# Kernel optimization log

Measured on AMD Instinct MI355X. Metric: run time of the kernel, lower is better.

The kernel has to match this reference:

```python
import jax, jax.numpy as jnp
import numpy as np

N_A = 100000
N_B = 100000


def _mean_agg(x_src, src, dst, n_dst):
    # gather source features along edges, mean-aggregate into destination nodes
    msgs = x_src[src]                                        # [E, d]
    s = jax.ops.segment_sum(msgs, dst, num_segments=n_dst)   # [n_dst, d]
    ones = jnp.ones((dst.shape[0], 1), dtype=x_src.dtype)
    cnt = jax.ops.segment_sum(ones, dst, num_segments=n_dst)
    return s / jnp.maximum(cnt, jnp.asarray(1.0, x_src.dtype))


def setup_inputs() -> dict:
    key = jax.random.key(0)
    ks = jax.random.split(key, 13)
    E = 1200000
    d = 64
    return {
        "x_A": jax.random.normal(ks[0], (N_A, d), jnp.float32),
        "x_B": jax.random.normal(ks[1], (N_B, d), jnp.float32),
        "Wn": jax.random.normal(ks[2], (2, 3, d, d), jnp.float32) * 0.1,
        "Wr": jax.random.normal(ks[3], (2, 3, d, d), jnp.float32) * 0.1,
        "b": jax.random.normal(ks[4], (2, 3, d), jnp.float32) * 0.1,
        "W_out": jax.random.normal(ks[5], (d, d), jnp.float32) * 0.1,
        "b_out": jax.random.normal(ks[6], (d,), jnp.float32) * 0.1,
        "src0": jax.random.randint(ks[7], (E,), 0, N_A, jnp.int64 if jax.config.jax_enable_x64 else jnp.int32),
        "dst0": jax.random.randint(ks[8], (E,), 0, N_B, jnp.int32),
        "src1": jax.random.randint(ks[9], (E,), 0, N_B, jnp.int32),
        "dst1": jax.random.randint(ks[10], (E,), 0, N_A, jnp.int32),
        "src2": jax.random.randint(ks[11], (E,), 0, N_A, jnp.int32),
        "dst2": jax.random.randint(ks[12], (E,), 0, N_A, jnp.int32),
    }


def reference(x_A, x_B, Wn, Wr, b, W_out, b_out,
              src0, dst0, src1, dst1, src2, dst2):
    # Two stacked heterogeneous conv layers (SAGEConv-style per edge type,
    # summed across edge types per destination node type), then Linear+ReLU head.
    for l in range(2):
        m0 = _mean_agg(x_A, src0, dst0, N_B)  # A -> B
        m1 = _mean_agg(x_B, src1, dst1, N_A)  # B -> A
        m2 = _mean_agg(x_A, src2, dst2, N_A)  # A -> A
        new_B = m0 @ Wn[l, 0] + x_B @ Wr[l, 0] + b[l, 0]
        new_A = (m1 @ Wn[l, 1] + x_A @ Wr[l, 1] + b[l, 1]
                 + m2 @ Wn[l, 2] + x_A @ Wr[l, 2] + b[l, 2])
        x_A, x_B = new_A, new_B
    out_A = jax.nn.relu(x_A @ W_out + b_out)
    out_B = jax.nn.relu(x_B @ W_out + b_out)
    return jnp.concatenate([out_A, out_B], axis=0)  # [N_A + N_B, d]
```

## Files before the change

kernel.cpp:

```cpp
#include <hip/hip_runtime.h>
#include <hip/hip_bf16.h>

typedef __bf16 bf16_t;
typedef unsigned short u16;
typedef short short8 __attribute__((ext_vector_type(8)));
typedef float f32x4 __attribute__((ext_vector_type(4)));

#define BSHIFT 9
#define CAP 8192
#define TILE 8192

__device__ inline short f2bs(float v) {
    bf16_t h = (bf16_t)v;
    return __builtin_bit_cast(short, h);
}
__device__ inline float uif(unsigned u) { return __builtin_bit_cast(float, u); }

__global__ __launch_bounds__(256) void prep_convert(
    const float* __restrict__ xA, const float* __restrict__ xB,
    const float* __restrict__ Wn, const float* __restrict__ Wr,
    const float* __restrict__ Wout, const float* __restrict__ b,
    const float* __restrict__ b_out,
    u16* __restrict__ plane0, u16* __restrict__ wh,
    int* __restrict__ gcursor, float* __restrict__ biasC,
    int NA, int NB, int K) {
    int nA4 = NA * 16, nB4 = NB * 16;
    int bA = (nA4 + 255) / 256, bB = (nB4 + 255) / 256;
    int bi = blockIdx.x;
    int tid = threadIdx.x;
    if (bi < bA + bB) {
        const float* in = (bi < bA) ? xA : xB;
        u16* out = (bi < bA) ? plane0 : plane0 + (size_t)NA * 64;
        int i = (bi < bA ? bi : bi - bA) * 256 + tid;
        int n4 = (bi < bA) ? nA4 : nB4;
        if (i >= n4) return;
        float4 v = ((const float4*)in)[i];
        u16 o[4];
        o[0] = (u16)f2bs(v.x); o[1] = (u16)f2bs(v.y);
        o[2] = (u16)f2bs(v.z); o[3] = (u16)f2bs(v.w);
        *(uint2*)(out + (size_t)i * 4) = *(uint2*)o;
        return;
    }
    if (bi < bA + bB + 11) {
        int mat = bi - bA - bB;
        u16* dstp = wh + (size_t)mat * 4096;
        for (int i = tid; i < 4096; i += 256) {
            int k = i >> 6, n = i & 63;
            float v;
            if (mat < 6) v = Wn[(size_t)mat * 4096 + i];
            else if (mat < 8) v = Wr[(size_t)((mat - 6) * 3 + 0) * 4096 + i];
            else if (mat < 10) v = Wr[(size_t)((mat - 8) * 3 + 1) * 4096 + i]
                                 + Wr[(size_t)((mat - 8) * 3 + 2) * 4096 + i];
            else v = Wout[i];
            dstp[n * 64 + k] = (u16)f2bs(v);
        }
        return;
    }
    if (bi < bA + bB + 11 + 5) {
        int c = bi - bA - bB - 11;
        const float* Wsrc;
        const float* Wsrc2 = nullptr;
        if (c == 0) Wsrc = Wn + (size_t)3 * 4096;
        else if (c == 1) Wsrc = Wr + (size_t)3 * 4096;
        else if (c == 2) Wsrc = Wn + (size_t)4 * 4096;
        else if (c == 3) Wsrc = Wn + (size_t)5 * 4096;
        else { Wsrc = Wr + (size_t)4 * 4096; Wsrc2 = Wr + (size_t)5 * 4096; }
        __shared__ float Ws[64 * 64];
        __shared__ float Wo[64 * 64];
        for (int i = tid; i < 4096; i += 256) {
            float w = Wsrc[i];
            if (Wsrc2) w += Wsrc2[i];
            Ws[i] = w;
            Wo[i] = Wout[i];
        }
        __syncthreads();
        u16* dstp = wh + (size_t)(11 + c) * 4096;
        for (int it = 0; it < 16; ++it) {
            int i = it * 256 + tid;
            int k = i >> 6, n = i & 63;
            float s0 = 0.f, s1 = 0.f, s2 = 0.f, s3 = 0.f;
#pragma unroll
            for (int j = 0; j < 64; j += 4) {
                s0 += Ws[k * 64 + j]     * Wo[j * 64 + n];
                s1 += Ws[k * 64 + j + 1] * Wo[(j + 1) * 64 + n];
                s2 += Ws[k * 64 + j + 2] * Wo[(j + 2) * 64 + n];
                s3 += Ws[k * 64 + j + 3] * Wo[(j + 3) * 64 + n];
            }
            dstp[n * 64 + k] = (u16)f2bs((s0 + s1) + (s2 + s3));
        }
        return;
    }
    for (int i = tid; i < K; i += 256) gcursor[i] = i * CAP;
    if (tid < 64) {
        int n = tid;
        float s0 = b_out[n], s1 = b_out[n];
        for (int j = 0; j < 64; j++) {
            float wo = Wout[j * 64 + n];
            s0 += b[3 * 64 + j] * wo;
            s1 += (b[4 * 64 + j] + b[5 * 64 + j]) * wo;
        }
        biasC[0 * 64 + n] = b[0 * 64 + n];
        biasC[1 * 64 + n] = b[1 * 64 + n] + b[2 * 64 + n];
        biasC[2 * 64 + n] = s0;
        biasC[3 * 64 + n] = s1;
    }
}

__global__ __launch_bounds__(1024) void partition_kernel(
    const int* __restrict__ s0, const int* __restrict__ d0,
    const int* __restrict__ s1, const int* __restrict__ d1,
    const int* __restrict__ s2, const int* __restrict__ d2,
    int* __restrict__ gcursor, int* __restrict__ pairs,
    int NB, int NA, int E, int total) {
    __shared__ int hist[1024];
    __shared__ int gbase[1024];
    int tid = threadIdx.x;
    for (int tile = blockIdx.x * TILE; tile < total; tile += gridDim.x * TILE) {
        hist[tid] = 0;
        __syncthreads();
        int mybkt[8], mypk[8], myrank[8];
#pragma unroll
        for (int j = 0; j < 8; j++) {
            int idx = tile + j * 1024 + tid;
            int g = -1, s = 0;
            if (idx < total) {
                if (idx < E) { s = s0[idx]; g = d0[idx]; }
                else if (idx < 2 * E) { s = s1[idx - E]; g = NB + d1[idx - E]; }
                else { s = s2[idx - 2 * E]; g = NB + NA + d2[idx - 2 * E]; }
            }
            if (g >= 0) {
                mybkt[j] = g >> BSHIFT;
                mypk[j] = ((g & ((1 << BSHIFT) - 1)) << 17) | s;
                myrank[j] = atomicAdd(&hist[mybkt[j]], 1);
            } else mybkt[j] = -1;
        }
        __syncthreads();
        {
            int c = hist[tid];
            if (c) gbase[tid] = atomicAdd(&gcursor[tid], c);
        }
        __syncthreads();
#pragma unroll
        for (int j = 0; j < 8; j++) {
            if (mybkt[j] >= 0)
                pairs[gbase[mybkt[j]] + myrank[j]] = mypk[j];
        }
        __syncthreads();
    }
}

__global__ __launch_bounds__(512) void bucket_fill(const int* __restrict__ pairs,
                                                   const int* __restrict__ gcursor,
                                                   int* __restrict__ off_s,
                                                   int* __restrict__ off_e,
                                                   int* __restrict__ colidx, int M) {
    int b = blockIdx.x;
    int gb = b << BSHIFT;
    __shared__ int cnt[512], cur[512], wsum[8];
    int tid = threadIdx.x;
    int lane = tid & 63, w = tid >> 6;
    int p0 = b * CAP, p1 = gcursor[b];
    cnt[tid] = 0;
    __syncthreads();
    for (int e = p0 + tid; e < p1; e += 512)
        atomicAdd(&cnt[(unsigned)pairs[e] >> 17], 1);
    __syncthreads();
    int v = cnt[tid];
    int x = v;
#pragma unroll
    for (int off = 1; off < 64; off <<= 1) {
        int n = __shfl_up(x, off);
        if (lane >= off) x += n;
    }
    if (lane == 63) wsum[w] = x;
    __syncthreads();
    if (tid == 0) {
        int s = 0;
#pragma unroll
        for (int i = 0; i < 8; i++) { int t = wsum[i]; wsum[i] = s; s += t; }
    }
    __syncthreads();
    int excl = x - v + wsum[w];
    cur[tid] = excl;
    int g = gb + tid;
    if (g < M) { off_s[g] = p0 + excl; off_e[g] = p0 + excl + v; }
    __syncthreads();
    for (int e = p0 + tid; e < p1; e += 512) {
        int p = pairs[e];
        int pos = atomicAdd(&cur[(unsigned)p >> 17], 1);
        colidx[p0 + pos] = p & 0x1FFFF;
    }
}

__device__ __forceinline__ void acc8(uint4 u, f32x4& a0, f32x4& a1) {
    a0[0] += uif(u.x << 16); a0[1] += uif(u.x & 0xFFFF0000u);
    a0[2] += uif(u.y << 16); a0[3] += uif(u.y & 0xFFFF0000u);
    a1[0] += uif(u.z << 16); a1[1] += uif(u.z & 0xFFFF0000u);
    a1[2] += uif(u.w << 16); a1[3] += uif(u.w & 0xFFFF0000u);
}

__device__ __forceinline__ uint4 gather_seg(const char* __restrict__ tab,
                                            const int* __restrict__ colidx,
                                            int s0, int s1, unsigned fo) {
    f32x4 a0 = {0.f, 0.f, 0.f, 0.f}, a1 = {0.f, 0.f, 0.f, 0.f};
    int e = s0;
    if (e + 3 < s1) {
        int c0 = colidx[e], c1 = colidx[e + 1];
        int c2 = colidx[e + 2], c3 = colidx[e + 3];
        while (e + 7 < s1) {
            uint4 u0 = *(const uint4*)(tab + (((unsigned)c0 << 7) | fo));
            uint4 u1 = *(const uint4*)(tab + (((unsigned)c1 << 7) | fo));
            uint4 u2 = *(const uint4*)(tab + (((unsigned)c2 << 7) | fo));
            uint4 u3 = *(const uint4*)(tab + (((unsigned)c3 << 7) | fo));
            c0 = colidx[e + 4]; c1 = colidx[e + 5];
            c2 = colidx[e + 6]; c3 = colidx[e + 7];
            acc8(u0, a0, a1); acc8(u1, a0, a1);
            acc8(u2, a0, a1); acc8(u3, a0, a1);
            e += 4;
        }
        {
            uint4 u0 = *(const uint4*)(tab + (((unsigned)c0 << 7) | fo));
            uint4 u1 = *(const uint4*)(tab + (((unsigned)c1 << 7) | fo));
            uint4 u2 = *(const uint4*)(tab + (((unsigned)c2 << 7) | fo));
            uint4 u3 = *(const uint4*)(tab + (((unsigned)c3 << 7) | fo));
            acc8(u0, a0, a1); acc8(u1, a0, a1);
            acc8(u2, a0, a1); acc8(u3, a0, a1);
            e += 4;
        }
    }
    for (; e < s1; ++e) {
        int c = colidx[e];
        uint4 u = *(const uint4*)(tab + (((unsigned)c << 7) | fo));
        acc8(u, a0, a1);
    }
    float inv = 1.0f / fmaxf((float)(s1 - s0), 1.0f);
    u16 o[8];
#pragma unroll
    for (int i = 0; i < 4; i++) o[i] = (u16)f2bs(a0[i] * inv);
#pragma unroll
    for (int i = 0; i < 4; i++) o[4 + i] = (u16)f2bs(a1[i] * inv);
    return *(uint4*)o;
}

template <int L2>
__global__ __launch_bounds__(256) void fused_layer(
    const u16* __restrict__ plane_in, void* __restrict__ outv,
    const int* __restrict__ colidx,
    const int* __restrict__ off_s, const int* __restrict__ off_e,
    const u16* __restrict__ wh, const float* __restrict__ biasC,
    int NA, int NB, int blocksBf) {
    __shared__ __align__(16) u16 mS[32][72];
    const int tid = threadIdx.x;
    const int w = tid >> 6, lane = tid & 63;
    const int oct = lane >> 3, fl = lane & 7;
    const unsigned fo = (unsigned)(fl << 4);
    const char* pA = (const char*)plane_in;
    const char* pB = (const char*)(plane_in + (size_t)NA * 64);
    const int r = lane & 15, q = lane >> 4;
    short8 zf;
#pragma unroll
    for (int j = 0; j < 8; j++) zf[j] = 0;

    if ((int)blockIdx.x < blocksBf) {
        const int row0 = blockIdx.x * 32;
        const int rt = w >> 1;
        const int tbase = (w & 1) * 2;
        const int arow = row0 + rt * 16 + r;
        const bool av = arow < NB;
        short8 ax0 = av ? *(const short8*)(pB + (size_t)arow * 128 + q * 16) : zf;
        short8 ax1 = av ? *(const short8*)(pB + (size_t)arow * 128 + 64 + q * 16) : zf;
        {
            int seg = w * 8 + oct;
            int brow = row0 + seg;
            int s0 = 0, s1 = 0;
            if (brow < NB) { s0 = off_s[brow]; s1 = off_e[brow]; }
            uint4 mv = gather_seg(pA, colidx, s0, s1, fo);
            *(uint4*)&mS[seg][fl * 8] = mv;
        }
        __syncthreads();
        const u16* WmT = wh + (size_t)(L2 ? 11 : 0) * 4096;
        const u16* WxT = wh + (size_t)(L2 ? 12 : 6) * 4096;
        const float* bb = biasC + (size_t)(L2 ? 2 : 0) * 64;
        f32x4 acc[2];
#pragma unroll
        for (int t2 = 0; t2 < 2; t2++) {
            float bv = bb[(tbase + t2) * 16 + r];
            acc[t2][0] = bv; acc[t2][1] = bv; acc[t2][2] = bv; acc[t2][3] = bv;
        }
#pragma unroll
        for (int ks = 0; ks < 2; ks++) {
            short8 am = *(const short8*)&mS[rt * 16 + r][ks * 32 + q * 8];
            short8 ax = ks ? ax1 : ax0;
#pragma unroll
            for (int t2 = 0; t2 < 2; t2++) {
                size_t widx = (size_t)((tbase + t2) * 16 + r) * 64 + ks * 32 + q * 8;
                acc[t2] = __builtin_amdgcn_mfma_f32_16x16x32_bf16(am, *(const short8*)(WmT + widx), acc[t2], 0, 0, 0);
                acc[t2] = __builtin_amdgcn_mfma_f32_16x16x32_bf16(ax, *(const short8*)(WxT + widx), acc[t2], 0, 0, 0);
            }
        }
#pragma unroll
        for (int t2 = 0; t2 < 2; t2++) {
            int col = (tbase + t2) * 16 + r;
#pragma unroll
            for (int rr = 0; rr < 4; rr++) {
                int row = row0 + rt * 16 + q * 4 + rr;
                if (row < NB) {
                    float v = acc[t2][rr];
                    if (L2) __builtin_nontemporal_store(fmaxf(v, 0.0f),
                                (float*)outv + (size_t)(NA + row) * 64 + col);
                    else ((u16*)outv)[(size_t)(NA + row) * 64 + col] = (u16)f2bs(v);
                }
            }
        }
    } else {
        const int row0 = ((int)blockIdx.x - blocksBf) * 16;
        const int t = w;
        const int arow = row0 + r;
        const bool av = arow < NA;
        short8 ax0 = av ? *(const short8*)(pA + (size_t)arow * 128 + q * 16) : zf;
        short8 ax1 = av ? *(const short8*)(pA + (size_t)arow * 128 + 64 + q * 16) : zf;
        {
            int seg = w * 8 + oct;
            int rrow = row0 + (seg & 15);
            bool m2 = seg >= 16;
            int s0 = 0, s1 = 0;
            if (rrow < NA) {
                int g = m2 ? (NB + NA + rrow) : (NB + rrow);
                s0 = off_s[g]; s1 = off_e[g];
            }
            uint4 mv = gather_seg(m2 ? pA : pB, colidx, s0, s1, fo);
            *(uint4*)&mS[seg][fl * 8] = mv;
        }
        __syncthreads();
        const u16* Wm1T = wh + (size_t)(L2 ? 13 : 1) * 4096;
        const u16* Wm2T = wh + (size_t)(L2 ? 14 : 2) * 4096;
        const u16* WxT  = wh + (size_t)(L2 ? 15 : 8) * 4096;
        const float* bb = biasC + (size_t)(L2 ? 3 : 1) * 64;
        f32x4 acc;
        {
            float bv = bb[t * 16 + r];
            acc[0] = bv; acc[1] = bv; acc[2] = bv; acc[3] = bv;
        }
#pragma unroll
        for (int ks = 0; ks < 2; ks++) {
            short8 am1 = *(const short8*)&mS[r][ks * 32 + q * 8];
            short8 am2 = *(const short8*)&mS[16 + r][ks * 32 + q * 8];
            short8 ax = ks ? ax1 : ax0;
            size_t widx = (size_t)(t * 16 + r) * 64 + ks * 32 + q * 8;
            acc = __builtin_amdgcn_mfma_f32_16x16x32_bf16(am1, *(const short8*)(Wm1T + widx), acc, 0, 0, 0);
            acc = __builtin_amdgcn_mfma_f32_16x16x32_bf16(am2, *(const short8*)(Wm2T + widx), acc, 0, 0, 0);
            acc = __builtin_amdgcn_mfma_f32_16x16x32_bf16(ax, *(const short8*)(WxT + widx), acc, 0, 0, 0);
        }
        {
            int col = t * 16 + r;
#pragma unroll
            for (int rr = 0; rr < 4; rr++) {
                int row = row0 + q * 4 + rr;
                if (row < NA) {
                    float v = acc[rr];
                    if (L2) __builtin_nontemporal_store(fmaxf(v, 0.0f),
                                (float*)outv + (size_t)row * 64 + col);
                    else ((u16*)outv)[(size_t)row * 64 + col] = (u16)f2bs(v);
                }
            }
        }
    }
}

extern "C" void kernel_launch(void* const* d_in, const int* in_sizes, int n_in,
                              void* d_out, int out_size, void* d_ws, size_t ws_size,
                              hipStream_t stream) {
    const float* xA_in = (const float*)d_in[0];
    const float* xB_in = (const float*)d_in[1];
    const float* Wn = (const float*)d_in[2];
    const float* Wr = (const float*)d_in[3];
    const float* b = (const float*)d_in[4];
    const float* W_out = (const float*)d_in[5];
    const float* b_out = (const float*)d_in[6];
    const int* src0 = (const int*)d_in[7];
    const int* dst0 = (const int*)d_in[8];
    const int* src1 = (const int*)d_in[9];
    const int* dst1 = (const int*)d_in[10];
    const int* src2 = (const int*)d_in[11];
    const int* dst2 = (const int*)d_in[12];

    const int NA = in_sizes[0] / 64;
    const int NB = in_sizes[1] / 64;
    const int E = in_sizes[7];
    const int M = NB + NA + NA;
    const int total = 3 * E;
    const int K = (M + (1 << BSHIFT) - 1) >> BSHIFT;

    const size_t PL = (size_t)(NA + NB) * 64;
    u16* plane[2];
    plane[0] = (u16*)d_ws;
    plane[1] = plane[0] + PL;
    u16* wh     = plane[1] + PL;
    int* gcursor= (int*)(wh + 16 * 4096);
    float* biasC= (float*)(gcursor + 1024);
    int* off_s  = (int*)(biasC + 256);
    int* off_e  = off_s + M;
    int* colidx = off_e + M;
    int* pairs  = colidx + (size_t)K * CAP;

    int bA = (NA * 16 + 255) / 256, bB = (NB * 16 + 255) / 256;
    prep_convert<<<bA + bB + 11 + 5 + 1, 256, 0, stream>>>(
        xA_in, xB_in, Wn, Wr, W_out, b, b_out,
        plane[0], wh, gcursor, biasC, NA, NB, K);

    int ntiles = (total + TILE - 1) / TILE;
    partition_kernel<<<ntiles, 1024, 0, stream>>>(src0, dst0, src1, dst1, src2, dst2,
                                                  gcursor, pairs, NB, NA, E, total);
    bucket_fill<<<K, 512, 0, stream>>>(pairs, gcursor, off_s, off_e, colidx, M);

    const int blocksBf = (NB + 31) / 32;
    const int blocksAf = (NA + 15) / 16;
    fused_layer<0><<<blocksBf + blocksAf, 256, 0, stream>>>(
        plane[0], plane[1], colidx, off_s, off_e, wh, biasC, NA, NB, blocksBf);
    fused_layer<1><<<blocksBf + blocksAf, 256, 0, stream>>>(
        plane[1], d_out, colidx, off_s, off_e, wh, biasC, NA, NB, blocksBf);
}
```

Baseline: 379.2 us.

## Merge edge partitioning into the prep kernel with smaller tiles

The edge-bucket partition kernel is folded into the input-conversion/weight-prep kernel as extra blocks, so partitioning and feature conversion run concurrently in one launch. Partition tiles shrink from 8192 edges with 1024 threads to 2048 edges with 256 threads. Bucket cursors become relative counts zeroed by a memset instead of being initialized in the prep kernel, which removes the ordering dependency between the two. The smaller tiles mean more global atomics on the cursors, and a memset launch is added to the stream.

```diff
diff --git a/kernel.cpp b/kernel.cpp
--- a/kernel.cpp
+++ b/kernel.cpp
@@ -8,7 +8,7 @@
 
 #define BSHIFT 9
 #define CAP 8192
-#define TILE 8192
+#define PTILE 2048
 
 __device__ inline short f2bs(float v) {
     bf16_t h = (bf16_t)v;
@@ -16,18 +16,61 @@
 }
 __device__ inline float uif(unsigned u) { return __builtin_bit_cast(float, u); }
 
-__global__ __launch_bounds__(256) void prep_convert(
+__global__ __launch_bounds__(256) void mega_prep_partition(
     const float* __restrict__ xA, const float* __restrict__ xB,
     const float* __restrict__ Wn, const float* __restrict__ Wr,
     const float* __restrict__ Wout, const float* __restrict__ b,
     const float* __restrict__ b_out,
+    const int* __restrict__ s0, const int* __restrict__ d0,
+    const int* __restrict__ s1, const int* __restrict__ d1,
+    const int* __restrict__ s2, const int* __restrict__ d2,
     u16* __restrict__ plane0, u16* __restrict__ wh,
     int* __restrict__ gcursor, float* __restrict__ biasC,
-    int NA, int NB, int K) {
+    int* __restrict__ pairs,
+    int NA, int NB, int E, int total, int ntiles) {
+    __shared__ __align__(16) char smem[32768];
+    int bi = blockIdx.x;
+    int tid = threadIdx.x;
+
+    if (bi < ntiles) {
+        int* hist = (int*)smem;
+        int* gbase = hist + 1024;
+        for (int i = tid; i < 1024; i += 256) hist[i] = 0;
+        __syncthreads();
+        int tile = bi * PTILE;
+        int mybkt[8], mypk[8], myrank[8];
+#pragma unroll
+        for (int j = 0; j < 8; j++) {
+            int idx = tile + j * 256 + tid;
+            int g = -1, s = 0;
+            if (idx < total) {
+                if (idx < E) { s = s0[idx]; g = d0[idx]; }
+                else if (idx < 2 * E) { s = s1[idx - E]; g = NB + d1[idx - E]; }
+                else { s = s2[idx - 2 * E]; g = NB + NA + d2[idx - 2 * E]; }
+            }
+            if (g >= 0) {
+                mybkt[j] = g >> BSHIFT;
+                mypk[j] = ((g & ((1 << BSHIFT) - 1)) << 17) | s;
+                myrank[j] = atomicAdd(&hist[mybkt[j]], 1);
+            } else mybkt[j] = -1;
+        }
+        __syncthreads();
+        for (int bq = tid; bq < 1024; bq += 256) {
+            int c = hist[bq];
+            if (c) gbase[bq] = bq * CAP + atomicAdd(&gcursor[bq], c);
+        }
+        __syncthreads();
+#pragma unroll
+        for (int j = 0; j < 8; j++) {
+            if (mybkt[j] >= 0)
+                pairs[gbase[mybkt[j]] + myrank[j]] = mypk[j];
+        }
+        return;
+    }
+
+    bi -= ntiles;
     int nA4 = NA * 16, nB4 = NB * 16;
     int bA = (nA4 + 255) / 256, bB = (nB4 + 255) / 256;
-    int bi = blockIdx.x;
-    int tid = threadIdx.x;
     if (bi < bA + bB) {
         const float* in = (bi < bA) ? xA : xB;
         u16* out = (bi < bA) ? plane0 : plane0 + (size_t)NA * 64;
@@ -65,8 +108,8 @@
         else if (c == 2) Wsrc = Wn + (size_t)4 * 4096;
         else if (c == 3) Wsrc = Wn + (size_t)5 * 4096;
         else { Wsrc = Wr + (size_t)4 * 4096; Wsrc2 = Wr + (size_t)5 * 4096; }
-        __shared__ float Ws[64 * 64];
-        __shared__ float Wo[64 * 64];
+        float* Ws = (float*)smem;
+        float* Wo = Ws + 4096;
         for (int i = tid; i < 4096; i += 256) {
             float w = Wsrc[i];
             if (Wsrc2) w += Wsrc2[i];
@@ -78,74 +121,30 @@
         for (int it = 0; it < 16; ++it) {
             int i = it * 256 + tid;
             int k = i >> 6, n = i & 63;
-            float s0 = 0.f, s1 = 0.f, s2 = 0.f, s3 = 0.f;
+            float p0 = 0.f, p1 = 0.f, p2 = 0.f, p3 = 0.f;
 #pragma unroll
             for (int j = 0; j < 64; j += 4) {
-                s0 += Ws[k * 64 + j]     * Wo[j * 64 + n];
-                s1 += Ws[k * 64 + j + 1] * Wo[(j + 1) * 64 + n];
-                s2 += Ws[k * 64 + j + 2] * Wo[(j + 2) * 64 + n];
-                s3 += Ws[k * 64 + j + 3] * Wo[(j + 3) * 64 + n];
-            }
-            dstp[n * 64 + k] = (u16)f2bs((s0 + s1) + (s2 + s3));
+                p0 += Ws[k * 64 + j]     * Wo[j * 64 + n];
+                p1 += Ws[k * 64 + j + 1] * Wo[(j + 1) * 64 + n];
+                p2 += Ws[k * 64 + j + 2] * Wo[(j + 2) * 64 + n];
+                p3 += Ws[k * 64 + j + 3] * Wo[(j + 3) * 64 + n];
+            }
+            dstp[n * 64 + k] = (u16)f2bs((p0 + p1) + (p2 + p3));
         }
         return;
     }
-    for (int i = tid; i < K; i += 256) gcursor[i] = i * CAP;
     if (tid < 64) {
         int n = tid;
-        float s0 = b_out[n], s1 = b_out[n];
+        float s0v = b_out[n], s1v = b_out[n];
         for (int j = 0; j < 64; j++) {
             float wo = Wout[j * 64 + n];
-            s0 += b[3 * 64 + j] * wo;
-            s1 += (b[4 * 64 + j] + b[5 * 64 + j]) * wo;
+            s0v += b[3 * 64 + j] * wo;
+            s1v += (b[4 * 64 + j] + b[5 * 64 + j]) * wo;
         }
         biasC[0 * 64 + n] = b[0 * 64 + n];
         biasC[1 * 64 + n] = b[1 * 64 + n] + b[2 * 64 + n];
-        biasC[2 * 64 + n] = s0;
-        biasC[3 * 64 + n] = s1;
-    }
-}
-
-__global__ __launch_bounds__(1024) void partition_kernel(
-    const int* __restrict__ s0, const int* __restrict__ d0,
-    const int* __restrict__ s1, const int* __restrict__ d1,
-    const int* __restrict__ s2, const int* __restrict__ d2,
-    int* __restrict__ gcursor, int* __restrict__ pairs,
-    int NB, int NA, int E, int total) {
-    __shared__ int hist[1024];
-    __shared__ int gbase[1024];
-    int tid = threadIdx.x;
-    for (int tile = blockIdx.x * TILE; tile < total; tile += gridDim.x * TILE) {
-        hist[tid] = 0;
-        __syncthreads();
-        int mybkt[8], mypk[8], myrank[8];
-#pragma unroll
-        for (int j = 0; j < 8; j++) {
-            int idx = tile + j * 1024 + tid;
-            int g = -1, s = 0;
-            if (idx < total) {
-                if (idx < E) { s = s0[idx]; g = d0[idx]; }
-                else if (idx < 2 * E) { s = s1[idx - E]; g = NB + d1[idx - E]; }
-                else { s = s2[idx - 2 * E]; g = NB + NA + d2[idx - 2 * E]; }
-            }
-            if (g >= 0) {
-                mybkt[j] = g >> BSHIFT;
-                mypk[j] = ((g & ((1 << BSHIFT) - 1)) << 17) | s;
-                myrank[j] = atomicAdd(&hist[mybkt[j]], 1);
-            } else mybkt[j] = -1;
-        }
-        __syncthreads();
-        {
-            int c = hist[tid];
-            if (c) gbase[tid] = atomicAdd(&gcursor[tid], c);
-        }
-        __syncthreads();
-#pragma unroll
-        for (int j = 0; j < 8; j++) {
-            if (mybkt[j] >= 0)
-                pairs[gbase[mybkt[j]] + myrank[j]] = mypk[j];
-        }
-        __syncthreads();
+        biasC[2 * 64 + n] = s0v;
+        biasC[3 * 64 + n] = s1v;
     }
 }
 
@@ -159,7 +158,7 @@
     __shared__ int cnt[512], cur[512], wsum[8];
     int tid = threadIdx.x;
     int lane = tid & 63, w = tid >> 6;
-    int p0 = b * CAP, p1 = gcursor[b];
+    int p0 = b * CAP, p1 = p0 + gcursor[b];
     cnt[tid] = 0;
     __syncthreads();
     for (int e = p0 + tid; e < p1; e += 512)
@@ -404,13 +403,13 @@
     int* pairs  = colidx + (size_t)K * CAP;
 
     int bA = (NA * 16 + 255) / 256, bB = (NB * 16 + 255) / 256;
-    prep_convert<<<bA + bB + 11 + 5 + 1, 256, 0, stream>>>(
+    int ntiles = (total + PTILE - 1) / PTILE;
+    hipMemsetAsync(gcursor, 0, 1024 * 4, stream);
+    mega_prep_partition<<<ntiles + bA + bB + 11 + 5 + 1, 256, 0, stream>>>(
         xA_in, xB_in, Wn, Wr, W_out, b, b_out,
-        plane[0], wh, gcursor, biasC, NA, NB, K);
-
-    int ntiles = (total + TILE - 1) / TILE;
-    partition_kernel<<<ntiles, 1024, 0, stream>>>(src0, dst0, src1, dst1, src2, dst2,
-                                                  gcursor, pairs, NB, NA, E, total);
+        src0, dst0, src1, dst1, src2, dst2,
+        plane[0], wh, gcursor, biasC, pairs, NA, NB, E, total, ntiles);
+
     bucket_fill<<<K, 512, 0, stream>>>(pairs, gcursor, off_s, off_e, colidx, M);
 
     const int blocksBf = (NB + 31) / 32;
```

After: 398.4 us. 5.1% more time.
